# Kernel tuning notes

Hardware: AMD Instinct MI355X
Metric: run time of the kernel (lower is better)

Reference implementation:

```python
import jax, jax.numpy as jnp
import numpy as np

NH = 32
LN_EPS = 1e-5

def _mlp2(x, w1, b1, w2, b2):
    # Linear -> ReLU -> Linear (torch convention: y = x @ W^T + b)
    return jnp.maximum(x @ w1.T + b1, 0.0) @ w2.T + b2

def _layernorm(x, g, b):
    m = x.mean(-1, keepdims=True)
    v = jnp.mean((x - m) ** 2, axis=-1, keepdims=True)
    return (x - m) / jnp.sqrt(v + LN_EPS) * g + b

def _pos_enc(pos):
    # P[..., 2i] = sin(pos/(i+1)*pi), P[..., 2i+1] = cos(pos/(i+1)*pi)
    i = jnp.arange(NH // 2, dtype=pos.dtype)
    ang = pos[..., None] * (jnp.pi / (i + 1.0))  # [B, L, NH/2]
    return jnp.stack([jnp.sin(ang), jnp.cos(ang)], axis=-1).reshape(pos.shape[0], pos.shape[1], NH)

def _forward(x0, x1, pos0, pos1, xcT,
             e0w1, e0b1, e0w2, e0b2,
             e1w1, e1b1, e1w2, e1b2,
             ecw1, ecb1, ecw2, ecb2,
             wq, wk, wv, wo,
             ln1g, ln1b, ln2g, ln2b,
             f1w1, f1b1, f1w2, f1b2,
             f2w1, f2b1, f2w2, f2b2,
             l0, l1):
    # InputFeature
    e0 = _mlp2(x0, e0w1, e0b1, e0w2, e0b2) + _pos_enc(pos0)      # [B, l0, 32]
    e1 = _mlp2(x1, e1w1, e1b1, e1w2, e1b2) + _pos_enc(pos1)      # [B, l1, 32]
    ec = _mlp2(xcT, ecw1, ecb1, ecw2, ecb2)                      # [B, 32]
    xIn = jnp.concatenate([e0, e1, ec[:, None, :]], axis=1)      # [B, L, 32], L = l0+l1+1
    # AttentionLayer: attention over the feature axis (faithful to bmm(q^T, k))
    q = xIn @ wq.T; k = xIn @ wk.T; v = xIn @ wv.T               # [B, L, 32]
    L = xIn.shape[1]
    score = jnp.einsum('blh,blg->bhg', q, k) / jnp.sqrt(jnp.asarray(L, xIn.dtype))  # [B, 32, 32]
    att = jax.nn.softmax(score, axis=-1)
    a = jnp.einsum('bhg,blg->blh', att, v) @ wo.T                # [B, L, 32]
    # addnorm1 (dropout in eval = identity) + ffn1 + addnorm2 + ffn2
    h1 = _layernorm(a + xIn, ln1g, ln1b)
    h2 = _mlp2(h1, f1w1, f1b1, f1w2, f1b2)
    h3 = _layernorm(h2 + xIn, ln2g, ln2b)
    y = _mlp2(h3, f2w1, f2b1, f2w2, f2b2)[..., 0]                # [B, L]
    # segment-mean pooling: sum of per-segment means (last segment = xc token)
    return y[:, :l0].mean(-1) + y[:, l0:l0 + l1].mean(-1) + y[:, l0 + l1:].mean(-1)

def setup_inputs() -> dict:
    key = jax.random.key(0)
    ks = iter(jax.random.split(key, 48))
    B, L0, L1, N0, N1, NXC = 2048, 365, 366, 8, 16, 32
    lin = lambda o, i: jax.random.normal(next(ks), (o, i), jnp.float32) * np.float32(1.0 / np.sqrt(i))
    d = {}
    d['x0'] = jax.random.normal(next(ks), (B, L0, N0), jnp.float32)
    d['x1'] = jax.random.normal(next(ks), (B, L1, N1), jnp.float32)
    d['pos0'] = jax.random.uniform(next(ks), (B, L0), jnp.float32) * 365.0
    d['pos1'] = jax.random.uniform(next(ks), (B, L1), jnp.float32) * 365.0
    d['xcT'] = jax.random.normal(next(ks), (B, NXC), jnp.float32)
    d['e0w1'] = lin(NH, N0); d['e0b1'] = jnp.zeros((NH,), jnp.float32)
    d['e0w2'] = lin(NH, NH); d['e0b2'] = jnp.zeros((NH,), jnp.float32)
    d['e1w1'] = lin(NH, N1); d['e1b1'] = jnp.zeros((NH,), jnp.float32)
    d['e1w2'] = lin(NH, NH); d['e1b2'] = jnp.zeros((NH,), jnp.float32)
    d['ecw1'] = lin(NH, NXC); d['ecb1'] = jnp.zeros((NH,), jnp.float32)
    d['ecw2'] = lin(NH, NH); d['ecb2'] = jnp.zeros((NH,), jnp.float32)
    d['wq'] = lin(NH, NH); d['wk'] = lin(NH, NH); d['wv'] = lin(NH, NH); d['wo'] = lin(NH, NH)
    d['ln1g'] = jnp.ones((NH,), jnp.float32); d['ln1b'] = jnp.zeros((NH,), jnp.float32)
    d['ln2g'] = jnp.ones((NH,), jnp.float32); d['ln2b'] = jnp.zeros((NH,), jnp.float32)
    d['f1w1'] = lin(NH, NH); d['f1b1'] = jnp.zeros((NH,), jnp.float32)
    d['f1w2'] = lin(NH, NH); d['f1b2'] = jnp.zeros((NH,), jnp.float32)
    d['f2w1'] = lin(NH, NH); d['f2b1'] = jnp.zeros((NH,), jnp.float32)
    d['f2w2'] = lin(1, NH); d['f2b2'] = jnp.zeros((1,), jnp.float32)
    d['l0'] = L0; d['l1'] = L1
    return d

def reference(x0, x1, pos0, pos1, xcT,
              e0w1, e0b1, e0w2, e0b2, e1w1, e1b1, e1w2, e1b2,
              ecw1, ecb1, ecw2, ecb2, wq, wk, wv, wo,
              ln1g, ln1b, ln2g, ln2b,
              f1w1, f1b1, f1w2, f1b2, f2w1, f2b1, f2w2, f2b2,
              l0, l1):
    return _forward(x0, x1, pos0, pos1, xcT,
                    e0w1, e0b1, e0w2, e0b2, e1w1, e1b1, e1w2, e1b2,
                    ecw1, ecb1, ecw2, ecb2, wq, wk, wv, wo,
                    ln1g, ln1b, ln2g, ln2b,
                    f1w1, f1b1, f1w2, f1b2, f2w1, f2b1, f2w2, f2b2,
                    l0, l1)
```

## Files before the change

kernel.cpp:

```cpp
#include <hip/hip_runtime.h>
#include <math.h>

#define L0T 365
#define L1T 366
#define LT  732
#define NTILE 46
#define NSEG 23
#define NW   4
#define NTHR 256

#define SB_NO_DS 0x7F

typedef short svec8 __attribute__((ext_vector_type(8)));
typedef float fvec4 __attribute__((ext_vector_type(4)));
typedef float fvec16 __attribute__((ext_vector_type(16)));
typedef unsigned uvec4 __attribute__((ext_vector_type(4)));

__device__ __forceinline__ unsigned short f2bf(float f) {
    unsigned u = __float_as_uint(f);
    u = (u + 0x7fffu + ((u >> 16) & 1u)) >> 16;
    return (unsigned short)u;
}
__device__ __forceinline__ float bf2f(unsigned short s) {
    return __uint_as_float(((unsigned)s) << 16);
}
__device__ __forceinline__ unsigned pk2(float a, float b) {
    return (unsigned)f2bf(a) | ((unsigned)f2bf(b) << 16);
}
__device__ __forceinline__ unsigned cvtpk(float a, float b) {
    unsigned r;
    asm("v_cvt_pk_bf16_f32 %0, %1, %2" : "=v"(r) : "v"(a), "v"(b));
    return r;
}
__device__ __forceinline__ float pgetv(uvec4 p, int j) {
    unsigned u = p[j >> 1];
    return bf2f((unsigned short)((j & 1) ? (u >> 16) : (u & 0xffffu)));
}
__device__ __forceinline__ svec8 pack8(float4 a, float4 c) {
    uvec4 u;
    u[0] = cvtpk(a.x, a.y); u[1] = cvtpk(a.z, a.w);
    u[2] = cvtpk(c.x, c.y); u[3] = cvtpk(c.z, c.w);
    return __builtin_bit_cast(svec8, u);
}
__device__ __forceinline__ void fastsc(float rev, float& s, float& c) {
    float fr;
    asm("v_fract_f32 %0, %1" : "=v"(fr) : "v"(rev));
    asm("v_sin_f32 %0, %1"   : "=v"(s)  : "v"(fr));
    asm("v_cos_f32 %0, %1"   : "=v"(c)  : "v"(fr));
}
__device__ __forceinline__ svec8 ldfrag(const unsigned short* p) {
    asm volatile("" : "+v"(p));
    return *(const svec8*)p;
}

__device__ __forceinline__ void embed_pass(
    const unsigned short* __restrict__ T1,
    const unsigned short* __restrict__ T2,
    const float* __restrict__ Bh, const float* __restrict__ Bx,
    svec8 bx, int ln, int Q, float* __restrict__ out)
{
    svec8 w1f0 = *(const svec8*)&T1[ln * 8];
    svec8 w1f1 = *(const svec8*)&T1[512 + ln * 8];
    const fvec4* bh = (const fvec4*)&Bh[Q * 8];
    fvec4 d0 = __builtin_amdgcn_mfma_f32_16x16x32_bf16(w1f0, bx, bh[0], 0, 0, 0);
    fvec4 d1 = __builtin_amdgcn_mfma_f32_16x16x32_bf16(w1f1, bx, bh[1], 0, 0, 0);
    uvec4 hu;
    hu[0] = cvtpk(fmaxf(d0[0], 0.f), fmaxf(d0[1], 0.f));
    hu[1] = cvtpk(fmaxf(d0[2], 0.f), fmaxf(d0[3], 0.f));
    hu[2] = cvtpk(fmaxf(d1[0], 0.f), fmaxf(d1[1], 0.f));
    hu[3] = cvtpk(fmaxf(d1[2], 0.f), fmaxf(d1[3], 0.f));
    svec8 hf = __builtin_bit_cast(svec8, hu);
    svec8 w2f0 = *(const svec8*)&T2[ln * 8];
    svec8 w2f1 = *(const svec8*)&T2[512 + ln * 8];
    const fvec4* bb = (const fvec4*)&Bx[Q * 8];
    fvec4 g0 = __builtin_amdgcn_mfma_f32_16x16x32_bf16(w2f0, hf, bb[0], 0, 0, 0);
    fvec4 g1 = __builtin_amdgcn_mfma_f32_16x16x32_bf16(w2f1, hf, bb[1], 0, 0, 0);
    out[0] = g0[0]; out[1] = g0[1]; out[2] = g0[2]; out[3] = g0[3];
    out[4] = g1[0]; out[5] = g1[1]; out[6] = g1[2]; out[7] = g1[3];
}

__device__ __forceinline__ void load_tile(
    int t, int b, int tk, int Q,
    const float* __restrict__ x0, const float* __restrict__ x1,
    const float* __restrict__ pos0, const float* __restrict__ pos1,
    svec8& bx, float& pv, int& seg, int& tl)
{
    seg = (t >= NSEG) ? 1 : 0;
    tl  = (seg ? (t - NSEG) : t) * 16 + tk;
    const int lim = seg ? L1T : L0T;
    const bool tvalid = tl < lim;
    #pragma unroll
    for (int j = 0; j < 8; j++) bx[j] = 0;
    const bool ld = tvalid && (seg ? (Q < 2) : (Q == 0));
    if (ld) {
        const float4* px = seg
            ? (const float4*)(x1 + ((size_t)b * L1T + tl) * 16 + Q * 8)
            : (const float4*)(x0 + ((size_t)b * L0T + tl) * 8);
        bx = pack8(px[0], px[1]);
    }
    pv = 0.f;
    if (tvalid) pv = seg ? pos1[(size_t)b * L1T + tl] : pos0[(size_t)b * L0T + tl];
}

__device__ __forceinline__ void finish_xv(
    int seg, int tl, int Q, const float* __restrict__ e, float pv, float4 pwr,
    const float* __restrict__ ECV, float* __restrict__ xv)
{
    const int lim = seg ? L1T : L0T;
    const bool tvalid = tl < lim;
    const bool isxc = seg && (tl == L1T);
    const float pwa[4] = {pwr.x, pwr.y, pwr.z, pwr.w};
    #pragma unroll
    for (int j = 0; j < 8; j += 2) {
        float s, c; fastsc(pv * pwa[j >> 1], s, c);
        float a0 = e[j] + s, a1 = e[j + 1] + c;
        xv[j]     = tvalid ? a0 : (isxc ? ECV[Q * 8 + j]     : 0.f);
        xv[j + 1] = tvalid ? a1 : (isxc ? ECV[Q * 8 + j + 1] : 0.f);
    }
}

__global__ __launch_bounds__(NTHR, 8) void embed_gram_kernel(
    const float* __restrict__ x0,  const float* __restrict__ x1,
    const float* __restrict__ pos0,const float* __restrict__ pos1,
    const float* __restrict__ xcT,
    const float* __restrict__ e0w1,const float* __restrict__ e0b1,
    const float* __restrict__ e0w2,const float* __restrict__ e0b2,
    const float* __restrict__ e1w1,const float* __restrict__ e1b1,
    const float* __restrict__ e1w2,const float* __restrict__ e1b2,
    const float* __restrict__ ecw1,const float* __restrict__ ecb1,
    const float* __restrict__ ecw2,const float* __restrict__ ecb2,
    const float* __restrict__ wq,  const float* __restrict__ wk,
    const float* __restrict__ wv,  const float* __restrict__ wo,
    unsigned short* __restrict__ wsWb, float* __restrict__ wsEC)
{
    const int b   = blockIdx.x;
    const int tid = threadIdx.x;
    const int w   = tid >> 6;
    const int ln  = tid & 63;
    const int tk  = ln & 15;
    const int Q   = ln >> 4;

    __shared__ unsigned short TBL[4 * 1024] __attribute__((aligned(16)));
    __shared__ float BIA[128] __attribute__((aligned(16)));
    __shared__ unsigned short SCB[2304] __attribute__((aligned(16)));
    __shared__ float Cm[1024] __attribute__((aligned(16)));
    __shared__ float ECV[32] __attribute__((aligned(16)));

    float* T1f = (float*)SCB;

    float4 pwr;
    pwr.x = 0.5f / (float)(Q * 4 + 1);
    pwr.y = 0.5f / (float)(Q * 4 + 2);
    pwr.z = 0.5f / (float)(Q * 4 + 3);
    pwr.w = 0.5f / (float)(Q * 4 + 4);

    for (int idx = tid; idx < 1024; idx += NTHR) {
        int f = idx >> 9, lane = (idx >> 3) & 63, j = idx & 7;
        int tkk = lane & 15, QQ = lane >> 4;
        int Lr = ((tkk >> 2) * 8) + (tkk & 3) + f * 4;
        int col = QQ * 8 + j;
        TBL[idx]        = (col < 8)  ? f2bf(e0w1[Lr * 8  + col]) : (unsigned short)0;
        TBL[1024 + idx] = f2bf(e0w2[Lr * 32 + col]);
        TBL[2048 + idx] = (col < 16) ? f2bf(e1w1[Lr * 16 + col]) : (unsigned short)0;
        TBL[3072 + idx] = f2bf(e1w2[Lr * 32 + col]);
        Cm[idx] = 0.f;
    }
    if (tid < 128) {
        int s = tid >> 5, i = tid & 31;
        float bv;
        if      (s == 0) bv = e0b1[i];
        else if (s == 1) bv = e0b2[i];
        else if (s == 2) bv = e1b1[i];
        else             bv = e1b2[i];
        BIA[tid] = bv;
    }
    float* ECH = T1f;
    if (tid >= 224) {
        int i = tid - 224;
        const float4* xr = (const float4*)(xcT + (size_t)b * 32);
        const float4* wr = (const float4*)&ecw1[i * 32];
        float a = ecb1[i];
        #pragma unroll
        for (int j4 = 0; j4 < 8; j4++) {
            float4 ww = wr[j4], xx = xr[j4];
            a = fmaf(ww.x, xx.x, a); a = fmaf(ww.y, xx.y, a);
            a = fmaf(ww.z, xx.z, a); a = fmaf(ww.w, xx.w, a);
        }
        ECH[i] = fmaxf(a, 0.f);
    }
    __syncthreads();
    if (tid >= 224) {
        int i = tid - 224;
        const float4* wr = (const float4*)&ecw2[i * 32];
        float a = ecb2[i];
        #pragma unroll
        for (int j4 = 0; j4 < 8; j4++) {
            float4 ww = wr[j4];
            a = fmaf(ww.x, ECH[j4 * 4 + 0], a); a = fmaf(ww.y, ECH[j4 * 4 + 1], a);
            a = fmaf(ww.z, ECH[j4 * 4 + 2], a); a = fmaf(ww.w, ECH[j4 * 4 + 3], a);
        }
        ECV[i] = a;
        wsEC[(size_t)b * 32 + i] = a;
    }
    __syncthreads();

    {
        const int feat = ln & 31, half = ln >> 5;
        const int wbase = w * 576;
        const int waddr = wbase + tk * 32 + (tk >> 3) * 32 + Q * 8;
        const int rbase = wbase + half * 288 + feat;
        fvec16 dG;
        #pragma unroll
        for (int i = 0; i < 16; i++) dG[i] = 0.f;
        for (int t = w; t < NTILE; t += NW) {
            svec8 bx; float pv; int sg, tl;
            load_tile(t, b, tk, Q, x0, x1, pos0, pos1, bx, pv, sg, tl);
            float e[8];
            {
                const unsigned short* T = TBL + sg * 2048;
                const float* Bb = BIA + sg * 64;
                embed_pass(T, T + 1024, Bb, Bb + 32, bx, ln, Q, e);
            }
            float xv[8]; finish_xv(sg, tl, Q, e, pv, pwr, ECV, xv);
            uvec4 pk;
            pk[0] = cvtpk(xv[0], xv[1]); pk[1] = cvtpk(xv[2], xv[3]);
            pk[2] = cvtpk(xv[4], xv[5]); pk[3] = cvtpk(xv[6], xv[7]);
            __builtin_amdgcn_sched_barrier(SB_NO_DS);
            *(uvec4*)&SCB[waddr] = pk;
            __builtin_amdgcn_sched_barrier(SB_NO_DS);
            svec8 af;
            #pragma unroll
            for (int j = 0; j < 8; j++)
                af[j] = (short)SCB[rbase + j * 32];
            __builtin_amdgcn_sched_barrier(SB_NO_DS);
            dG = __builtin_amdgcn_mfma_f32_32x32x16_bf16(af, af, dG, 0, 0, 0);
        }
        #pragma unroll
        for (int rg = 0; rg < 16; rg++) {
            int row = (rg & 3) + 8 * (rg >> 2) + 4 * half;
            atomicAdd(&Cm[row * 32 + feat], dG[rg]);
        }
    }
    __syncthreads();

    for (int idx = tid; idx < 1024; idx += NTHR) {
        int i = idx >> 5, g = idx & 31;
        const float4* cr = (const float4*)&Cm[i * 32];
        const float4* wr = (const float4*)&wk[g * 32];
        float a = 0.f;
        #pragma unroll
        for (int j4 = 0; j4 < 8; j4++) {
            float4 cc = cr[j4], ww = wr[j4];
            a = fmaf(cc.x, ww.x, a); a = fmaf(cc.y, ww.y, a);
            a = fmaf(cc.z, ww.z, a); a = fmaf(cc.w, ww.w, a);
        }
        T1f[idx] = a;
    }
    __syncthreads();
    const float rsL = rsqrtf((float)LT);
    for (int idx = tid; idx < 1024; idx += NTHR) {
        int h = idx >> 5, g = idx & 31;
        const float4* qr = (const float4*)&wq[h * 32];
        float a = 0.f;
        #pragma unroll
        for (int i4 = 0; i4 < 8; i4++) {
            float4 qq = qr[i4];
            a = fmaf(qq.x, T1f[(i4 * 4 + 0) * 32 + g], a);
            a = fmaf(qq.y, T1f[(i4 * 4 + 1) * 32 + g], a);
            a = fmaf(qq.z, T1f[(i4 * 4 + 2) * 32 + g], a);
            a = fmaf(qq.w, T1f[(i4 * 4 + 3) * 32 + g], a);
        }
        Cm[idx] = a * rsL;
    }
    __syncthreads();
    {
        int r = tid >> 3, c0 = (tid & 7) * 4;
        float4 vv = *(const float4*)&Cm[r * 32 + c0];
        float m = fmaxf(fmaxf(vv.x, vv.y), fmaxf(vv.z, vv.w));
        m = fmaxf(m, __shfl_xor(m, 1));
        m = fmaxf(m, __shfl_xor(m, 2));
        m = fmaxf(m, __shfl_xor(m, 4));
        float ex = __expf(vv.x - m), ey = __expf(vv.y - m);
        float ez = __expf(vv.z - m), ew = __expf(vv.w - m);
        float s = ex + ey + ez + ew;
        s += __shfl_xor(s, 1); s += __shfl_xor(s, 2); s += __shfl_xor(s, 4);
        float inv = 1.f / s;
        float4 o; o.x = ex * inv; o.y = ey * inv; o.z = ez * inv; o.w = ew * inv;
        *(float4*)&Cm[r * 32 + c0] = o;
    }
    __syncthreads();
    for (int idx = tid; idx < 1024; idx += NTHR) {
        int h = idx >> 5, j = idx & 31;
        const float4* pr = (const float4*)&Cm[h * 32];
        float a = 0.f;
        #pragma unroll
        for (int g4 = 0; g4 < 8; g4++) {
            float4 pp = pr[g4];
            a = fmaf(pp.x, wv[(g4 * 4 + 0) * 32 + j], a);
            a = fmaf(pp.y, wv[(g4 * 4 + 1) * 32 + j], a);
            a = fmaf(pp.z, wv[(g4 * 4 + 2) * 32 + j], a);
            a = fmaf(pp.w, wv[(g4 * 4 + 3) * 32 + j], a);
        }
        T1f[idx] = a;
    }
    __syncthreads();
    for (int idx = tid; idx < 1024; idx += NTHR) {
        int o = idx >> 5, j = idx & 31;
        const float4* orow = (const float4*)&wo[o * 32];
        float a = 0.f;
        #pragma unroll
        for (int h4 = 0; h4 < 8; h4++) {
            float4 oo = orow[h4];
            a = fmaf(oo.x, T1f[(h4 * 4 + 0) * 32 + j], a);
            a = fmaf(oo.y, T1f[(h4 * 4 + 1) * 32 + j], a);
            a = fmaf(oo.z, T1f[(h4 * 4 + 2) * 32 + j], a);
            a = fmaf(oo.w, T1f[(h4 * 4 + 3) * 32 + j], a);
        }
        wsWb[(size_t)b * 1024 + idx] = f2bf(a + (o == j ? 1.f : 0.f));
    }
}

__global__ __launch_bounds__(NTHR, 8) void pipeline_kernel(
    const float* __restrict__ x0,  const float* __restrict__ x1,
    const float* __restrict__ pos0,const float* __restrict__ pos1,
    const float* __restrict__ e0w1,const float* __restrict__ e0b1,
    const float* __restrict__ e0w2,const float* __restrict__ e0b2,
    const float* __restrict__ e1w1,const float* __restrict__ e1b1,
    const float* __restrict__ e1w2,const float* __restrict__ e1b2,
    const float* __restrict__ ln1g,const float* __restrict__ ln1b,
    const float* __restrict__ ln2g,const float* __restrict__ ln2b,
    const float* __restrict__ f1w1,const float* __restrict__ f1b1,
    const float* __restrict__ f1w2,const float* __restrict__ f1b2,
    const float* __restrict__ f2w1,const float* __restrict__ f2b1,
    const float* __restrict__ f2w2,const float* __restrict__ f2b2,
    const unsigned short* __restrict__ wsWb, const float* __restrict__ wsEC,
    float* __restrict__ out)
{
    const int b   = blockIdx.x;
    const int tid = threadIdx.x;
    const int w   = tid >> 6;
    const int ln  = tid & 63;
    const int tk  = ln & 15;
    const int Q   = ln >> 4;

    __shared__ unsigned short TBL[4 * 1024] __attribute__((aligned(16)));
    __shared__ unsigned short WTB[4 * 1024] __attribute__((aligned(16)));
    __shared__ float BIA[128] __attribute__((aligned(16)));
    __shared__ unsigned PCK[128] __attribute__((aligned(16)));
    __shared__ float ECV[32] __attribute__((aligned(16)));
    __shared__ float red[NW * 3];

    float4 pwr;
    pwr.x = 0.5f / (float)(Q * 4 + 1);
    pwr.y = 0.5f / (float)(Q * 4 + 2);
    pwr.z = 0.5f / (float)(Q * 4 + 3);
    pwr.w = 0.5f / (float)(Q * 4 + 4);

    for (int idx = tid; idx < 1024; idx += NTHR) {
        int f = idx >> 9, lane = (idx >> 3) & 63, j = idx & 7;
        int tkk = lane & 15, QQ = lane >> 4;
        int Lr = ((tkk >> 2) * 8) + (tkk & 3) + f * 4;
        int col = QQ * 8 + j;
        TBL[idx]        = (col < 8)  ? f2bf(e0w1[Lr * 8  + col]) : (unsigned short)0;
        TBL[1024 + idx] = f2bf(e0w2[Lr * 32 + col]);
        TBL[2048 + idx] = (col < 16) ? f2bf(e1w1[Lr * 16 + col]) : (unsigned short)0;
        TBL[3072 + idx] = f2bf(e1w2[Lr * 32 + col]);
    }
    for (int idx = tid; idx < 4096; idx += NTHR) {
        int f = idx >> 9, lane = (idx >> 3) & 63, j = idx & 7;
        int tkk = lane & 15, QQ = lane >> 4;
        int Lr = ((tkk >> 2) * 8) + (tkk & 3) + (f & 1) * 4;
        int col = QQ * 8 + j;
        int wsel = f >> 1;
        unsigned short vbf;
        if      (wsel == 0) vbf = wsWb[(size_t)b * 1024 + Lr * 32 + col];
        else if (wsel == 1) vbf = f2bf(f1w1[Lr * 32 + col]);
        else if (wsel == 2) vbf = f2bf(f1w2[Lr * 32 + col]);
        else                vbf = f2bf(f2w1[Lr * 32 + col]);
        WTB[idx] = vbf;
    }
    if (tid < 128) {
        int s = tid >> 5, i = tid & 31;
        float bv;
        if      (s == 0) bv = e0b1[i];
        else if (s == 1) bv = e0b2[i];
        else if (s == 2) bv = e1b1[i];
        else             bv = e1b2[i];
        BIA[tid] = bv;
    }
    if (tid < 128) {
        int t8 = tid >> 4, q = (tid >> 2) & 3, i = tid & 3, f = q * 8 + 2 * i;
        const float* sp;
        if      (t8 == 0) sp = ln1g;
        else if (t8 == 1) sp = ln1b;
        else if (t8 == 2) sp = ln2g;
        else if (t8 == 3) sp = ln2b;
        else if (t8 == 4) sp = f1b1;
        else if (t8 == 5) sp = f1b2;
        else if (t8 == 6) sp = f2b1;
        else              sp = f2w2;
        PCK[tid] = pk2(sp[f], sp[f + 1]);
    }
    if (tid < 32) ECV[tid] = wsEC[(size_t)b * 32 + tid];
    __syncthreads();

    const float ybias = f2b2[0];
    const fvec4 zc = {0.f, 0.f, 0.f, 0.f};
    const uvec4* P4 = (const uvec4*)PCK;

    float s0 = 0.f, s1 = 0.f, s2 = 0.f;
    for (int t = w; t < NTILE; t += NW) {
        svec8 bx0; float pv; int sg, tl;
        load_tile(t, b, tk, Q, x0, x1, pos0, pos1, bx0, pv, sg, tl);
        float e[8];
        {
            const unsigned short* T = TBL + sg * 2048;
            const float* Bb = BIA + sg * 64;
            embed_pass(T, T + 1024, Bb, Bb + 32, bx0, ln, Q, e);
        }
        float xv[8]; finish_xv(sg, tl, Q, e, pv, pwr, ECV, xv);
        uvec4 pkx;
        pkx[0] = cvtpk(xv[0], xv[1]); pkx[1] = cvtpk(xv[2], xv[3]);
        pkx[2] = cvtpk(xv[4], xv[5]); pkx[3] = cvtpk(xv[6], xv[7]);
        svec8 bx = __builtin_bit_cast(svec8, pkx);

        svec8 wb0 = ldfrag(&WTB[ln * 8]);
        svec8 wb1 = ldfrag(&WTB[512 + ln * 8]);
        fvec4 d0 = __builtin_amdgcn_mfma_f32_16x16x32_bf16(wb0, bx, zc, 0, 0, 0);
        fvec4 d1 = __builtin_amdgcn_mfma_f32_16x16x32_bf16(wb1, bx, zc, 0, 0, 0);
        float v[8];
        #pragma unroll
        for (int j = 0; j < 4; j++) { v[j] = d0[j]; v[4 + j] = d1[j]; }
        float S = 0.f, Sq = 0.f;
        #pragma unroll
        for (int j = 0; j < 8; j++) { S += v[j]; Sq = fmaf(v[j], v[j], Sq); }
        S  += __shfl_xor(S, 16);  Sq += __shfl_xor(Sq, 16);
        S  += __shfl_xor(S, 32);  Sq += __shfl_xor(Sq, 32);
        float mean = S * (1.f / 32.f);
        float var = fmaxf(Sq * (1.f / 32.f) - mean * mean, 0.f);
        float rs = rsqrtf(var + 1e-5f);
        uvec4 pg1 = P4[Q], pb1 = P4[4 + Q];
        float n[8];
        #pragma unroll
        for (int j = 0; j < 8; j++)
            n[j] = (v[j] - mean) * rs * pgetv(pg1, j) + pgetv(pb1, j);
        uvec4 tu;
        tu[0] = cvtpk(n[0], n[1]); tu[1] = cvtpk(n[2], n[3]);
        tu[2] = cvtpk(n[4], n[5]); tu[3] = cvtpk(n[6], n[7]);
        svec8 tf = __builtin_bit_cast(svec8, tu);
        svec8 a1f0 = ldfrag(&WTB[1024 + ln * 8]);
        svec8 a1f1 = ldfrag(&WTB[1536 + ln * 8]);
        fvec4 u0 = __builtin_amdgcn_mfma_f32_16x16x32_bf16(a1f0, tf, zc, 0, 0, 0);
        fvec4 u1 = __builtin_amdgcn_mfma_f32_16x16x32_bf16(a1f1, tf, zc, 0, 0, 0);
        uvec4 pc1 = P4[16 + Q];
        uvec4 uu;
        uu[0] = cvtpk(fmaxf(u0[0] + pgetv(pc1, 0), 0.f), fmaxf(u0[1] + pgetv(pc1, 1), 0.f));
        uu[1] = cvtpk(fmaxf(u0[2] + pgetv(pc1, 2), 0.f), fmaxf(u0[3] + pgetv(pc1, 3), 0.f));
        uu[2] = cvtpk(fmaxf(u1[0] + pgetv(pc1, 4), 0.f), fmaxf(u1[1] + pgetv(pc1, 5), 0.f));
        uu[3] = cvtpk(fmaxf(u1[2] + pgetv(pc1, 6), 0.f), fmaxf(u1[3] + pgetv(pc1, 7), 0.f));
        svec8 uf = __builtin_bit_cast(svec8, uu);
        svec8 a2f0 = ldfrag(&WTB[2048 + ln * 8]);
        svec8 a2f1 = ldfrag(&WTB[2560 + ln * 8]);
        fvec4 g0 = __builtin_amdgcn_mfma_f32_16x16x32_bf16(a2f0, uf, zc, 0, 0, 0);
        fvec4 g1 = __builtin_amdgcn_mfma_f32_16x16x32_bf16(a2f1, uf, zc, 0, 0, 0);
        uvec4 pc2 = P4[20 + Q];
        #pragma unroll
        for (int j = 0; j < 8; j++)
            v[j] = (j < 4 ? g0[j] : g1[j - 4]) + pgetv(pc2, j) + xv[j];
        float S2 = 0.f, Sq2 = 0.f;
        #pragma unroll
        for (int j = 0; j < 8; j++) { S2 += v[j]; Sq2 = fmaf(v[j], v[j], Sq2); }
        S2  += __shfl_xor(S2, 16);  Sq2 += __shfl_xor(Sq2, 16);
        S2  += __shfl_xor(S2, 32);  Sq2 += __shfl_xor(Sq2, 32);
        float mean2 = S2 * (1.f / 32.f);
        float var2 = fmaxf(Sq2 * (1.f / 32.f) - mean2 * mean2, 0.f);
        float rs2 = rsqrtf(var2 + 1e-5f);
        uvec4 pg2 = P4[8 + Q], pb2 = P4[12 + Q];
        float n2[8];
        #pragma unroll
        for (int j = 0; j < 8; j++)
            n2[j] = (v[j] - mean2) * rs2 * pgetv(pg2, j) + pgetv(pb2, j);
        uvec4 t2u;
        t2u[0] = cvtpk(n2[0], n2[1]); t2u[1] = cvtpk(n2[2], n2[3]);
        t2u[2] = cvtpk(n2[4], n2[5]); t2u[3] = cvtpk(n2[6], n2[7]);
        svec8 t2 = __builtin_bit_cast(svec8, t2u);
        svec8 a3f0 = ldfrag(&WTB[3072 + ln * 8]);
        svec8 a3f1 = ldfrag(&WTB[3584 + ln * 8]);
        fvec4 q0 = __builtin_amdgcn_mfma_f32_16x16x32_bf16(a3f0, t2, zc, 0, 0, 0);
        fvec4 q1 = __builtin_amdgcn_mfma_f32_16x16x32_bf16(a3f1, t2, zc, 0, 0, 0);
        uvec4 pc3 = P4[24 + Q], pw2 = P4[28 + Q];
        float yp = 0.f;
        #pragma unroll
        for (int j = 0; j < 8; j++) {
            float ee = (j < 4 ? q0[j] : q1[j - 4]) + pgetv(pc3, j);
            yp = fmaf(pgetv(pw2, j), fmaxf(ee, 0.f), yp);
        }
        yp += __shfl_xor(yp, 16); yp += __shfl_xor(yp, 32);
        if (Q == 0) {
            float yv = yp + ybias;
            if (sg == 0) { if (tl < L0T) s0 += yv; }
            else {
                if (tl < L1T)       s1 += yv;
                else if (tl == L1T) s2 += yv;
            }
        }
    }

    s0 += __shfl_xor(s0, 1); s0 += __shfl_xor(s0, 2);
    s0 += __shfl_xor(s0, 4); s0 += __shfl_xor(s0, 8);
    s1 += __shfl_xor(s1, 1); s1 += __shfl_xor(s1, 2);
    s1 += __shfl_xor(s1, 4); s1 += __shfl_xor(s1, 8);
    s2 += __shfl_xor(s2, 1); s2 += __shfl_xor(s2, 2);
    s2 += __shfl_xor(s2, 4); s2 += __shfl_xor(s2, 8);
    if (ln == 0) { red[w * 3] = s0; red[w * 3 + 1] = s1; red[w * 3 + 2] = s2; }
    __syncthreads();
    if (tid == 0) {
        float a0 = 0.f, a1 = 0.f, a2 = 0.f;
        #pragma unroll
        for (int k = 0; k < NW; k++) {
            a0 += red[k * 3]; a1 += red[k * 3 + 1]; a2 += red[k * 3 + 2];
        }
        out[b] = a0 / (float)L0T + a1 / (float)L1T + a2;
    }
}

extern "C" void kernel_launch(void* const* d_in, const int* in_sizes, int n_in,
                              void* d_out, int out_size, void* d_ws, size_t ws_size,
                              hipStream_t stream)
{
    const float* x0   = (const float*)d_in[0];
    const float* x1   = (const float*)d_in[1];
    const float* pos0 = (const float*)d_in[2];
    const float* pos1 = (const float*)d_in[3];
    const float* xcT  = (const float*)d_in[4];
    const float* e0w1 = (const float*)d_in[5];
    const float* e0b1 = (const float*)d_in[6];
    const float* e0w2 = (const float*)d_in[7];
    const float* e0b2 = (const float*)d_in[8];
    const float* e1w1 = (const float*)d_in[9];
    const float* e1b1 = (const float*)d_in[10];
    const float* e1w2 = (const float*)d_in[11];
    const float* e1b2 = (const float*)d_in[12];
    const float* ecw1 = (const float*)d_in[13];
    const float* ecb1 = (const float*)d_in[14];
    const float* ecw2 = (const float*)d_in[15];
    const float* ecb2 = (const float*)d_in[16];
    const float* wq   = (const float*)d_in[17];
    const float* wk   = (const float*)d_in[18];
    const float* wv   = (const float*)d_in[19];
    const float* wo   = (const float*)d_in[20];
    const float* ln1g = (const float*)d_in[21];
    const float* ln1b = (const float*)d_in[22];
    const float* ln2g = (const float*)d_in[23];
    const float* ln2b = (const float*)d_in[24];
    const float* f1w1 = (const float*)d_in[25];
    const float* f1b1 = (const float*)d_in[26];
    const float* f1w2 = (const float*)d_in[27];
    const float* f1b2 = (const float*)d_in[28];
    const float* f2w1 = (const float*)d_in[29];
    const float* f2b1 = (const float*)d_in[30];
    const float* f2w2 = (const float*)d_in[31];
    const float* f2b2 = (const float*)d_in[32];
    float* out = (float*)d_out;

    const int B = in_sizes[0] / (L0T * 8);

    unsigned short* wsWb = (unsigned short*)d_ws;
    float* wsEC = (float*)((char*)d_ws + (size_t)B * 1024 * 2);

    hipLaunchKernelGGL(embed_gram_kernel, dim3(B), dim3(NTHR), 0, stream,
                       x0, x1, pos0, pos1, xcT,
                       e0w1, e0b1, e0w2, e0b2, e1w1, e1b1, e1w2, e1b2,
                       ecw1, ecb1, ecw2, ecb2, wq, wk, wv, wo,
                       wsWb, wsEC);
    hipLaunchKernelGGL(pipeline_kernel, dim3(B), dim3(NTHR), 0, stream,
                       x0, x1, pos0, pos1,
                       e0w1, e0b1, e0w2, e0b2, e1w1, e1b1, e1w2, e1b2,
                       ln1g, ln1b, ln2g, ln2b,
                       f1w1, f1b1, f1w2, f1b2, f2w1, f2b1, f2w2, f2b2,
                       wsWb, wsEC, out);
}
```

Baseline: 311.4 us.

## Cache embedded bf16 activations in workspace to skip re-embedding in second kernel

The first kernel now writes each tile's packed bf16 embedded input to a workspace buffer. A new lite pipeline kernel reads those packed values instead of reloading the raw inputs and recomputing the embedding MLP and positional encoding. The per-tile FFN/LayerNorm path is factored into a shared device function. The lite path is used only when the workspace is large enough; otherwise the original full kernel runs. This trades the recomputation for about 96 MB of extra global writes and reads.

After: 291.2 us. -6.5%, faster.

```diff
diff --git a/kernel.cpp b/kernel.cpp
--- a/kernel.cpp
+++ b/kernel.cpp
@@ -131,7 +131,8 @@
     const float* __restrict__ ecw2,const float* __restrict__ ecb2,
     const float* __restrict__ wq,  const float* __restrict__ wk,
     const float* __restrict__ wv,  const float* __restrict__ wo,
-    unsigned short* __restrict__ wsWb, float* __restrict__ wsEC)
+    unsigned short* __restrict__ wsWb, float* __restrict__ wsEC,
+    uvec4* __restrict__ wsX)
 {
     const int b   = blockIdx.x;
     const int tid = threadIdx.x;
@@ -225,6 +226,8 @@
             uvec4 pk;
             pk[0] = cvtpk(xv[0], xv[1]); pk[1] = cvtpk(xv[2], xv[3]);
             pk[2] = cvtpk(xv[4], xv[5]); pk[3] = cvtpk(xv[6], xv[7]);
+            if (wsX)
+                wsX[((size_t)b * NTILE + t) * 64 + tk * 4 + Q] = pk;
             __builtin_amdgcn_sched_barrier(SB_NO_DS);
             *(uvec4*)&SCB[waddr] = pk;
             __builtin_amdgcn_sched_barrier(SB_NO_DS);
@@ -320,7 +323,178 @@
     }
 }
 
-__global__ __launch_bounds__(NTHR, 8) void pipeline_kernel(
+__device__ __forceinline__ float pipe_tile(
+    uvec4 px, const unsigned short* __restrict__ WTB, const uvec4* __restrict__ P4,
+    int ln, int Q)
+{
+    const fvec4 zc = {0.f, 0.f, 0.f, 0.f};
+    svec8 bx = __builtin_bit_cast(svec8, px);
+    float xf[8];
+    #pragma unroll
+    for (int j = 0; j < 8; j++) xf[j] = pgetv(px, j);
+
+    svec8 wb0 = ldfrag(&WTB[ln * 8]);
+    svec8 wb1 = ldfrag(&WTB[512 + ln * 8]);
+    fvec4 d0 = __builtin_amdgcn_mfma_f32_16x16x32_bf16(wb0, bx, zc, 0, 0, 0);
+    fvec4 d1 = __builtin_amdgcn_mfma_f32_16x16x32_bf16(wb1, bx, zc, 0, 0, 0);
+    float v[8];
+    #pragma unroll
+    for (int j = 0; j < 4; j++) { v[j] = d0[j]; v[4 + j] = d1[j]; }
+    float S = 0.f, Sq = 0.f;
+    #pragma unroll
+    for (int j = 0; j < 8; j++) { S += v[j]; Sq = fmaf(v[j], v[j], Sq); }
+    S  += __shfl_xor(S, 16);  Sq += __shfl_xor(Sq, 16);
+    S  += __shfl_xor(S, 32);  Sq += __shfl_xor(Sq, 32);
+    float mean = S * (1.f / 32.f);
+    float var = fmaxf(Sq * (1.f / 32.f) - mean * mean, 0.f);
+    float rs = rsqrtf(var + 1e-5f);
+    uvec4 pg1 = P4[Q], pb1 = P4[4 + Q];
+    float n[8];
+    #pragma unroll
+    for (int j = 0; j < 8; j++)
+        n[j] = (v[j] - mean) * rs * pgetv(pg1, j) + pgetv(pb1, j);
+    uvec4 tu;
+    tu[0] = cvtpk(n[0], n[1]); tu[1] = cvtpk(n[2], n[3]);
+    tu[2] = cvtpk(n[4], n[5]); tu[3] = cvtpk(n[6], n[7]);
+    svec8 tf = __builtin_bit_cast(svec8, tu);
+    svec8 a1f0 = ldfrag(&WTB[1024 + ln * 8]);
+    svec8 a1f1 = ldfrag(&WTB[1536 + ln * 8]);
+    fvec4 u0 = __builtin_amdgcn_mfma_f32_16x16x32_bf16(a1f0, tf, zc, 0, 0, 0);
+    fvec4 u1 = __builtin_amdgcn_mfma_f32_16x16x32_bf16(a1f1, tf, zc, 0, 0, 0);
+    uvec4 pc1 = P4[16 + Q];
+    uvec4 uu;
+    uu[0] = cvtpk(fmaxf(u0[0] + pgetv(pc1, 0), 0.f), fmaxf(u0[1] + pgetv(pc1, 1), 0.f));
+    uu[1] = cvtpk(fmaxf(u0[2] + pgetv(pc1, 2), 0.f), fmaxf(u0[3] + pgetv(pc1, 3), 0.f));
+    uu[2] = cvtpk(fmaxf(u1[0] + pgetv(pc1, 4), 0.f), fmaxf(u1[1] + pgetv(pc1, 5), 0.f));
+    uu[3] = cvtpk(fmaxf(u1[2] + pgetv(pc1, 6), 0.f), fmaxf(u1[3] + pgetv(pc1, 7), 0.f));
+    svec8 uf = __builtin_bit_cast(svec8, uu);
+    svec8 a2f0 = ldfrag(&WTB[2048 + ln * 8]);
+    svec8 a2f1 = ldfrag(&WTB[2560 + ln * 8]);
+    fvec4 g0 = __builtin_amdgcn_mfma_f32_16x16x32_bf16(a2f0, uf, zc, 0, 0, 0);
+    fvec4 g1 = __builtin_amdgcn_mfma_f32_16x16x32_bf16(a2f1, uf, zc, 0, 0, 0);
+    uvec4 pc2 = P4[20 + Q];
+    #pragma unroll
+    for (int j = 0; j < 8; j++)
+        v[j] = (j < 4 ? g0[j] : g1[j - 4]) + pgetv(pc2, j) + xf[j];
+    float S2 = 0.f, Sq2 = 0.f;
+    #pragma unroll
+    for (int j = 0; j < 8; j++) { S2 += v[j]; Sq2 = fmaf(v[j], v[j], Sq2); }
+    S2  += __shfl_xor(S2, 16);  Sq2 += __shfl_xor(Sq2, 16);
+    S2  += __shfl_xor(S2, 32);  Sq2 += __shfl_xor(Sq2, 32);
+    float mean2 = S2 * (1.f / 32.f);
+    float var2 = fmaxf(Sq2 * (1.f / 32.f) - mean2 * mean2, 0.f);
+    float rs2 = rsqrtf(var2 + 1e-5f);
+    uvec4 pg2 = P4[8 + Q], pb2 = P4[12 + Q];
+    float n2[8];
+    #pragma unroll
+    for (int j = 0; j < 8; j++)
+        n2[j] = (v[j] - mean2) * rs2 * pgetv(pg2, j) + pgetv(pb2, j);
+    uvec4 t2u;
+    t2u[0] = cvtpk(n2[0], n2[1]); t2u[1] = cvtpk(n2[2], n2[3]);
+    t2u[2] = cvtpk(n2[4], n2[5]); t2u[3] = cvtpk(n2[6], n2[7]);
+    svec8 t2 = __builtin_bit_cast(svec8, t2u);
+    svec8 a3f0 = ldfrag(&WTB[3072 + ln * 8]);
+    svec8 a3f1 = ldfrag(&WTB[3584 + ln * 8]);
+    fvec4 q0 = __builtin_amdgcn_mfma_f32_16x16x32_bf16(a3f0, t2, zc, 0, 0, 0);
+    fvec4 q1 = __builtin_amdgcn_mfma_f32_16x16x32_bf16(a3f1, t2, zc, 0, 0, 0);
+    uvec4 pc3 = P4[24 + Q], pw2 = P4[28 + Q];
+    float yp = 0.f;
+    #pragma unroll
+    for (int j = 0; j < 8; j++) {
+        float ee = (j < 4 ? q0[j] : q1[j - 4]) + pgetv(pc3, j);
+        yp = fmaf(pgetv(pw2, j), fmaxf(ee, 0.f), yp);
+    }
+    yp += __shfl_xor(yp, 16); yp += __shfl_xor(yp, 32);
+    return yp;
+}
+
+__global__ __launch_bounds__(NTHR, 8) void pipeline_lite_kernel(
+    const float* __restrict__ ln1g,const float* __restrict__ ln1b,
+    const float* __restrict__ ln2g,const float* __restrict__ ln2b,
+    const float* __restrict__ f1w1,const float* __restrict__ f1b1,
+    const float* __restrict__ f1w2,const float* __restrict__ f1b2,
+    const float* __restrict__ f2w1,const float* __restrict__ f2b1,
+    const float* __restrict__ f2w2,const float* __restrict__ f2b2,
+    const unsigned short* __restrict__ wsWb, const uvec4* __restrict__ wsX,
+    float* __restrict__ out)
+{
+    const int b   = blockIdx.x;
+    const int tid = threadIdx.x;
+    const int w   = tid >> 6;
+    const int ln  = tid & 63;
+    const int tk  = ln & 15;
+    const int Q   = ln >> 4;
+
+    __shared__ unsigned short WTB[4 * 1024] __attribute__((aligned(16)));
+    __shared__ unsigned PCK[128] __attribute__((aligned(16)));
+    __shared__ float red[NW * 3];
+
+    for (int idx = tid; idx < 4096; idx += NTHR) {
+        int f = idx >> 9, lane = (idx >> 3) & 63, j = idx & 7;
+        int tkk = lane & 15, QQ = lane >> 4;
+        int Lr = ((tkk >> 2) * 8) + (tkk & 3) + (f & 1) * 4;
+        int col = QQ * 8 + j;
+        int wsel = f >> 1;
+        unsigned short vbf;
+        if      (wsel == 0) vbf = wsWb[(size_t)b * 1024 + Lr * 32 + col];
+        else if (wsel == 1) vbf = f2bf(f1w1[Lr * 32 + col]);
+        else if (wsel == 2) vbf = f2bf(f1w2[Lr * 32 + col]);
+        else                vbf = f2bf(f2w1[Lr * 32 + col]);
+        WTB[idx] = vbf;
+    }
+    if (tid < 128) {
+        int t8 = tid >> 4, q = (tid >> 2) & 3, i = tid & 3, f = q * 8 + 2 * i;
+        const float* sp;
+        if      (t8 == 0) sp = ln1g;
+        else if (t8 == 1) sp = ln1b;
+        else if (t8 == 2) sp = ln2g;
+        else if (t8 == 3) sp = ln2b;
+        else if (t8 == 4) sp = f1b1;
+        else if (t8 == 5) sp = f1b2;
+        else if (t8 == 6) sp = f2b1;
+        else              sp = f2w2;
+        PCK[tid] = pk2(sp[f], sp[f + 1]);
+    }
+    __syncthreads();
+
+    const float ybias = f2b2[0];
+    const uvec4* P4 = (const uvec4*)PCK;
+
+    float s0 = 0.f, s1 = 0.f, s2 = 0.f;
+    for (int t = w; t < NTILE; t += NW) {
+        uvec4 px = wsX[((size_t)b * NTILE + t) * 64 + tk * 4 + Q];
+        float yp = pipe_tile(px, WTB, P4, ln, Q);
+        if (Q == 0) {
+            const int sg = (t >= NSEG) ? 1 : 0;
+            const int tl = (sg ? (t - NSEG) : t) * 16 + tk;
+            float yv = yp + ybias;
+            if (sg == 0) { if (tl < L0T) s0 += yv; }
+            else {
+                if (tl < L1T)       s1 += yv;
+                else if (tl == L1T) s2 += yv;
+            }
+        }
+    }
+
+    s0 += __shfl_xor(s0, 1); s0 += __shfl_xor(s0, 2);
+    s0 += __shfl_xor(s0, 4); s0 += __shfl_xor(s0, 8);
+    s1 += __shfl_xor(s1, 1); s1 += __shfl_xor(s1, 2);
+    s1 += __shfl_xor(s1, 4); s1 += __shfl_xor(s1, 8);
+    s2 += __shfl_xor(s2, 1); s2 += __shfl_xor(s2, 2);
+    s2 += __shfl_xor(s2, 4); s2 += __shfl_xor(s2, 8);
+    if (ln == 0) { red[w * 3] = s0; red[w * 3 + 1] = s1; red[w * 3 + 2] = s2; }
+    __syncthreads();
+    if (tid == 0) {
+        float a0 = 0.f, a1 = 0.f, a2 = 0.f;
+        #pragma unroll
+        for (int k = 0; k < NW; k++) {
+            a0 += red[k * 3]; a1 += red[k * 3 + 1]; a2 += red[k * 3 + 2];
+        }
+        out[b] = a0 / (float)L0T + a1 / (float)L1T + a2;
+    }
+}
+
+__global__ __launch_bounds__(NTHR, 8) void pipeline_full_kernel(
     const float* __restrict__ x0,  const float* __restrict__ x1,
     const float* __restrict__ pos0,const float* __restrict__ pos1,
     const float* __restrict__ e0w1,const float* __restrict__ e0b1,
@@ -405,7 +579,6 @@
     __syncthreads();
 
     const float ybias = f2b2[0];
-    const fvec4 zc = {0.f, 0.f, 0.f, 0.f};
     const uvec4* P4 = (const uvec4*)PCK;
 
     float s0 = 0.f, s1 = 0.f, s2 = 0.f;
@@ -422,80 +595,7 @@
         uvec4 pkx;
         pkx[0] = cvtpk(xv[0], xv[1]); pkx[1] = cvtpk(xv[2], xv[3]);
         pkx[2] = cvtpk(xv[4], xv[5]); pkx[3] = cvtpk(xv[6], xv[7]);
-        svec8 bx = __builtin_bit_cast(svec8, pkx);
-
-        svec8 wb0 = ldfrag(&WTB[ln * 8]);
-        svec8 wb1 = ldfrag(&WTB[512 + ln * 8]);
-        fvec4 d0 = __builtin_amdgcn_mfma_f32_16x16x32_bf16(wb0, bx, zc, 0, 0, 0);
-        fvec4 d1 = __builtin_amdgcn_mfma_f32_16x16x32_bf16(wb1, bx, zc, 0, 0, 0);
-        float v[8];
-        #pragma unroll
-        for (int j = 0; j < 4; j++) { v[j] = d0[j]; v[4 + j] = d1[j]; }
-        float S = 0.f, Sq = 0.f;
-        #pragma unroll
-        for (int j = 0; j < 8; j++) { S += v[j]; Sq = fmaf(v[j], v[j], Sq); }
-        S  += __shfl_xor(S, 16);  Sq += __shfl_xor(Sq, 16);
-        S  += __shfl_xor(S, 32);  Sq += __shfl_xor(Sq, 32);
-        float mean = S * (1.f / 32.f);
-        float var = fmaxf(Sq * (1.f / 32.f) - mean * mean, 0.f);
-        float rs = rsqrtf(var + 1e-5f);
-        uvec4 pg1 = P4[Q], pb1 = P4[4 + Q];
-        float n[8];
-        #pragma unroll
-        for (int j = 0; j < 8; j++)
-            n[j] = (v[j] - mean) * rs * pgetv(pg1, j) + pgetv(pb1, j);
-        uvec4 tu;
-        tu[0] = cvtpk(n[0], n[1]); tu[1] = cvtpk(n[2], n[3]);
-        tu[2] = cvtpk(n[4], n[5]); tu[3] = cvtpk(n[6], n[7]);
-        svec8 tf = __builtin_bit_cast(svec8, tu);
-        svec8 a1f0 = ldfrag(&WTB[1024 + ln * 8]);
-        svec8 a1f1 = ldfrag(&WTB[1536 + ln * 8]);
-        fvec4 u0 = __builtin_amdgcn_mfma_f32_16x16x32_bf16(a1f0, tf, zc, 0, 0, 0);
-        fvec4 u1 = __builtin_amdgcn_mfma_f32_16x16x32_bf16(a1f1, tf, zc, 0, 0, 0);
-        uvec4 pc1 = P4[16 + Q];
-        uvec4 uu;
-        uu[0] = cvtpk(fmaxf(u0[0] + pgetv(pc1, 0), 0.f), fmaxf(u0[1] + pgetv(pc1, 1), 0.f));
-        uu[1] = cvtpk(fmaxf(u0[2] + pgetv(pc1, 2), 0.f), fmaxf(u0[3] + pgetv(pc1, 3), 0.f));
-        uu[2] = cvtpk(fmaxf(u1[0] + pgetv(pc1, 4), 0.f), fmaxf(u1[1] + pgetv(pc1, 5), 0.f));
-        uu[3] = cvtpk(fmaxf(u1[2] + pgetv(pc1, 6), 0.f), fmaxf(u1[3] + pgetv(pc1, 7), 0.f));
-        svec8 uf = __builtin_bit_cast(svec8, uu);
-        svec8 a2f0 = ldfrag(&WTB[2048 + ln * 8]);
-        svec8 a2f1 = ldfrag(&WTB[2560 + ln * 8]);
-        fvec4 g0 = __builtin_amdgcn_mfma_f32_16x16x32_bf16(a2f0, uf, zc, 0, 0, 0);
-        fvec4 g1 = __builtin_amdgcn_mfma_f32_16x16x32_bf16(a2f1, uf, zc, 0, 0, 0);
-        uvec4 pc2 = P4[20 + Q];
-        #pragma unroll
-        for (int j = 0; j < 8; j++)
-            v[j] = (j < 4 ? g0[j] : g1[j - 4]) + pgetv(pc2, j) + xv[j];
-        float S2 = 0.f, Sq2 = 0.f;
-        #pragma unroll
-        for (int j = 0; j < 8; j++) { S2 += v[j]; Sq2 = fmaf(v[j], v[j], Sq2); }
-        S2  += __shfl_xor(S2, 16);  Sq2 += __shfl_xor(Sq2, 16);
-        S2  += __shfl_xor(S2, 32);  Sq2 += __shfl_xor(Sq2, 32);
-        float mean2 = S2 * (1.f / 32.f);
-        float var2 = fmaxf(Sq2 * (1.f / 32.f) - mean2 * mean2, 0.f);
-        float rs2 = rsqrtf(var2 + 1e-5f);
-        uvec4 pg2 = P4[8 + Q], pb2 = P4[12 + Q];
-        float n2[8];
-        #pragma unroll
-        for (int j = 0; j < 8; j++)
-            n2[j] = (v[j] - mean2) * rs2 * pgetv(pg2, j) + pgetv(pb2, j);
-        uvec4 t2u;
-        t2u[0] = cvtpk(n2[0], n2[1]); t2u[1] = cvtpk(n2[2], n2[3]);
-        t2u[2] = cvtpk(n2[4], n2[5]); t2u[3] = cvtpk(n2[6], n2[7]);
-        svec8 t2 = __builtin_bit_cast(svec8, t2u);
-        svec8 a3f0 = ldfrag(&WTB[3072 + ln * 8]);
-        svec8 a3f1 = ldfrag(&WTB[3584 + ln * 8]);
-        fvec4 q0 = __builtin_amdgcn_mfma_f32_16x16x32_bf16(a3f0, t2, zc, 0, 0, 0);
-        fvec4 q1 = __builtin_amdgcn_mfma_f32_16x16x32_bf16(a3f1, t2, zc, 0, 0, 0);
-        uvec4 pc3 = P4[24 + Q], pw2 = P4[28 + Q];
-        float yp = 0.f;
-        #pragma unroll
-        for (int j = 0; j < 8; j++) {
-            float ee = (j < 4 ? q0[j] : q1[j - 4]) + pgetv(pc3, j);
-            yp = fmaf(pgetv(pw2, j), fmaxf(ee, 0.f), yp);
-        }
-        yp += __shfl_xor(yp, 16); yp += __shfl_xor(yp, 32);
+        float yp = pipe_tile(pkx, WTB, P4, ln, Q);
         if (Q == 0) {
             float yv = yp + ybias;
             if (sg == 0) { if (tl < L0T) s0 += yv; }
@@ -567,16 +667,27 @@
 
     unsigned short* wsWb = (unsigned short*)d_ws;
     float* wsEC = (float*)((char*)d_ws + (size_t)B * 1024 * 2);
+    size_t offX = (size_t)B * 1024 * 2 + (size_t)B * 32 * 4;
+    size_t needX = offX + (size_t)B * NTILE * 64 * 16;
+    const bool lite = (ws_size >= needX);
+    uvec4* wsX = lite ? (uvec4*)((char*)d_ws + offX) : (uvec4*)nullptr;
 
     hipLaunchKernelGGL(embed_gram_kernel, dim3(B), dim3(NTHR), 0, stream,
                        x0, x1, pos0, pos1, xcT,
                        e0w1, e0b1, e0w2, e0b2, e1w1, e1b1, e1w2, e1b2,
                        ecw1, ecb1, ecw2, ecb2, wq, wk, wv, wo,
-                       wsWb, wsEC);
-    hipLaunchKernelGGL(pipeline_kernel, dim3(B), dim3(NTHR), 0, stream,
-                       x0, x1, pos0, pos1,
-                       e0w1, e0b1, e0w2, e0b2, e1w1, e1b1, e1w2, e1b2,
-                       ln1g, ln1b, ln2g, ln2b,
-                       f1w1, f1b1, f1w2, f1b2, f2w1, f2b1, f2w2, f2b2,
-                       wsWb, wsEC, out);
-}
+                       wsWb, wsEC, wsX);
+    if (lite) {
+        hipLaunchKernelGGL(pipeline_lite_kernel, dim3(B), dim3(NTHR), 0, stream,
+                           ln1g, ln1b, ln2g, ln2b,
+                           f1w1, f1b1, f1w2, f1b2, f2w1, f2b1, f2w2, f2b2,
+                           wsWb, wsX, out);
+    } else {
+        hipLaunchKernelGGL(pipeline_full_kernel, dim3(B), dim3(NTHR), 0, stream,
+                           x0, x1, pos0, pos1,
+                           e0w1, e0b1, e0w2, e0b2, e1w1, e1b1, e1w2, e1b2,
+                           ln1g, ln1b, ln2g, ln2b,
+                           f1w1, f1b1, f1w2, f1b2, f2w1, f2b1, f2w2, f2b2,
+                           wsWb, wsEC, out);
+    }
+}
```
